# Kernel tuning notes

Hardware: AMD Instinct MI355X
Metric: run time of the kernel (lower is better)

## Reference

```python
import jax, jax.numpy as jnp
import numpy as np

B, N, D, H = 8, 1024, 512, 8
DH = D // H  # one_head_dim = 64


def setup_inputs() -> dict:
    key = jax.random.key(0)
    ks = jax.random.split(key, 7)
    s = 0.02
    return {
        "x": jax.random.normal(ks[0], (B, N, D), dtype=jnp.float32),
        "bias": jax.random.normal(ks[1], (B, N, N, H), dtype=jnp.float32),
        "Wq": jax.random.normal(ks[2], (D, D), dtype=jnp.float32) * s,
        "Wk": jax.random.normal(ks[3], (D, D), dtype=jnp.float32) * s,
        "Wv": jax.random.normal(ks[4], (D, D), dtype=jnp.float32) * s,
        "Wm": jax.random.normal(ks[5], (D, D), dtype=jnp.float32) * s,
        "bm": jnp.zeros((D,), dtype=jnp.float32),
    }


def reference(x, bias, Wq, Wk, Wv, Wm, bm):
    # Linear layers (torch Linear: y = x @ W.T); dropout is identity at eval.
    scale = DH ** -0.5
    q = (x @ Wq.T).reshape(B, N, H, DH).transpose(0, 2, 1, 3) * scale  # [B,H,N,DH]
    k = (x @ Wk.T).reshape(B, N, H, DH).transpose(0, 2, 1, 3)
    v = (x @ Wv.T).reshape(B, N, H, DH).transpose(0, 2, 1, 3)
    # scores + additive pairwise bias (bias permuted [B,N,N,H] -> [B,H,N,N])
    scores = jnp.einsum("bhnd,bhmd->bhnm", q, k) + bias.transpose(0, 3, 1, 2)
    attn = jax.nn.softmax(scores, axis=-1)
    out = jnp.einsum("bhnm,bhmd->bhnd", attn, v)  # [B,H,N,DH]
    out = out.transpose(0, 2, 1, 3).reshape(B, N, D)
    return out @ Wm.T + bm
```

## Files before the change

### kernel.cpp

```cpp
#include <hip/hip_runtime.h>
#include <hip/hip_bf16.h>

typedef __bf16 bf16x8 __attribute__((ext_vector_type(8)));
typedef __bf16 bf16x4 __attribute__((ext_vector_type(4)));
typedef float  f32x4  __attribute__((ext_vector_type(4)));

#define MFMA16(a, b, c) __builtin_amdgcn_mfma_f32_16x16x32_bf16((a), (b), (c), 0, 0, 0)

typedef const __attribute__((address_space(1))) unsigned int* gas_t;
typedef __attribute__((address_space(3))) unsigned int* las_t;
__device__ __forceinline__ void dma16(const __bf16* g, __bf16* l) {
    __builtin_amdgcn_global_load_lds((gas_t)g, (las_t)l, 16, 0, 0);
}


__global__ __launch_bounds__(256) void gemm_qkv(
    const float* __restrict__ x,
    const float* __restrict__ Wq, const float* __restrict__ Wk,
    const float* __restrict__ Wv,
    __bf16* __restrict__ qo, __bf16* __restrict__ ko, __bf16* __restrict__ vto)
{
    __shared__ __bf16 As[64][40];
    __shared__ __bf16 Bs[3][64][40];
    const int tid  = threadIdx.x;
    const int lane = tid & 63;
    const int wid  = tid >> 6;
    const int g    = lane >> 4, l16 = lane & 15;
    const int wr   = wid >> 1,  wc  = wid & 1;
    const int r0   = blockIdx.x * 64;
    const int c0   = blockIdx.y * 64;
    const float* Ws[3] = { Wq, Wk, Wv };

    const int sr  = tid >> 3;
    const int scq = tid & 7;

    f32x4 acc[3][2][2] = {};

    for (int k0 = 0; k0 < 512; k0 += 32) {
        __syncthreads();
#pragma unroll
        for (int j = 0; j < 2; ++j) {
            const int r = sr + 32 * j;
            float4 av = *reinterpret_cast<const float4*>(x + (size_t)(r0 + r) * 512 + k0 + scq * 4);
            bf16x4 ap = { (__bf16)av.x, (__bf16)av.y, (__bf16)av.z, (__bf16)av.w };
            *reinterpret_cast<bf16x4*>(&As[r][scq * 4]) = ap;
#pragma unroll
            for (int widx = 0; widx < 3; ++widx) {
                float4 bv = *reinterpret_cast<const float4*>(Ws[widx] + (size_t)(c0 + r) * 512 + k0 + scq * 4);
                bf16x4 bp = { (__bf16)bv.x, (__bf16)bv.y, (__bf16)bv.z, (__bf16)bv.w };
                *reinterpret_cast<bf16x4*>(&Bs[widx][r][scq * 4]) = bp;
            }
        }
        __syncthreads();
        bf16x8 af[2];
#pragma unroll
        for (int rt = 0; rt < 2; ++rt)
            af[rt] = *reinterpret_cast<const bf16x8*>(&As[wr * 32 + rt * 16 + l16][g * 8]);
#pragma unroll
        for (int widx = 0; widx < 3; ++widx) {
            bf16x8 bfr[2];
#pragma unroll
            for (int ct = 0; ct < 2; ++ct)
                bfr[ct] = *reinterpret_cast<const bf16x8*>(&Bs[widx][wc * 32 + ct * 16 + l16][g * 8]);
#pragma unroll
            for (int rt = 0; rt < 2; ++rt)
#pragma unroll
                for (int ct = 0; ct < 2; ++ct)
                    acc[widx][rt][ct] = MFMA16(af[rt], bfr[ct], acc[widx][rt][ct]);
        }
    }

#pragma unroll
    for (int widx = 0; widx < 2; ++widx) {
        __bf16* dst = (widx == 0) ? qo : ko;
        const float scale = (widx == 0) ? 0.125f : 1.0f;
#pragma unroll
        for (int rt = 0; rt < 2; ++rt)
#pragma unroll
            for (int ct = 0; ct < 2; ++ct)
#pragma unroll
                for (int reg = 0; reg < 4; ++reg) {
                    int r = r0 + wr * 32 + rt * 16 + 4 * g + reg;
                    int c = c0 + wc * 32 + ct * 16 + l16;
                    float val = acc[widx][rt][ct][reg] * scale;
                    int b = r >> 10, n = r & 1023, h = c >> 6, dh = c & 63;
                    dst[(((size_t)b * 8 + h) * 1024 + n) * 64 + dh] = (__bf16)val;
                }
    }
#pragma unroll
    for (int rt = 0; rt < 2; ++rt)
#pragma unroll
        for (int ct = 0; ct < 2; ++ct) {
            int r = r0 + wr * 32 + rt * 16 + 4 * g;
            int c = c0 + wc * 32 + ct * 16 + l16;
            int b = r >> 10, n = r & 1023, h = c >> 6, dh = c & 63;
            bf16x4 pv = { (__bf16)acc[2][rt][ct][0], (__bf16)acc[2][rt][ct][1],
                          (__bf16)acc[2][rt][ct][2], (__bf16)acc[2][rt][ct][3] };
            *reinterpret_cast<bf16x4*>(vto + (((size_t)b * 8 + h) * 64 + dh) * 1024 + n) = pv;
        }
}

__global__ __launch_bounds__(512, 2) void attn_v7(
    const __bf16* __restrict__ qw, const __bf16* __restrict__ kw,
    const __bf16* __restrict__ vtw, const float* __restrict__ bias,
    __bf16* __restrict__ ow)
{
    __shared__ __align__(16) __bf16 Ks[8][32][64];
    __shared__ __align__(16) __bf16 Vs[8][64][32];
    __shared__ __align__(16) __bf16 bsm[2][8][32][36];
    __shared__ __bf16 psm[8][32][40];
    const int tid  = threadIdx.x;
    const int w    = tid >> 6;
    const int lane = tid & 63;
    const int g    = lane >> 4, l16 = lane & 15;
    const int b    = blockIdx.x;
    const int n0   = blockIdx.y * 32;
    const size_t bhs = (size_t)b * 8 + w;

    const __bf16* kbase  = kw  + bhs * 1024 * 64;
    const __bf16* vbase  = vtw + bhs * 64 * 1024;
    const float*  bias_b = bias + ((size_t)(b * 1024 + n0)) * 8192;

    const int snr = tid >> 4;
    const int sf  = tid & 15;

    const int k_row  = lane >> 3;
    const int k_csrc = (lane & 7) ^ (k_row & 7);
    const int v_row  = lane >> 2;
    const int v_mc   = lane & 3;

    bf16x8 qf[2][2];
#pragma unroll
    for (int rf = 0; rf < 2; ++rf)
#pragma unroll
        for (int kc = 0; kc < 2; ++kc)
            qf[rf][kc] = *reinterpret_cast<const bf16x8*>(
                qw + (bhs * 1024 + n0 + rf * 16 + l16) * 64 + kc * 32 + g * 8);

    f32x4 o[2][4] = {};
    float lrun[2][4] = {};

    f32x4 bpA[4], bpB[4];

#define LOAD_BIAS(dst, tt)                                                     \
    {                                                                          \
        const int m0_ = (tt) * 32;                                             \
        _Pragma("unroll")                                                      \
        for (int c = 0; c < 4; ++c)                                            \
            dst[c] = __builtin_nontemporal_load(reinterpret_cast<const f32x4*>(\
                bias_b + (size_t)snr * 8192 + m0_ * 8 + (sf + 16 * c) * 4));   \
    }

#define WRITE_BIAS(buf, src)                                                   \
    {                                                                          \
        _Pragma("unroll")                                                      \
        for (int c = 0; c < 4; ++c) {                                          \
            const int f4 = sf + 16 * c;                                        \
            const int mm = f4 >> 1, h0 = (f4 & 1) * 4;                         \
            bsm[buf][h0 + 0][mm][snr] = (__bf16)src[c].x;                      \
            bsm[buf][h0 + 1][mm][snr] = (__bf16)src[c].y;                      \
            bsm[buf][h0 + 2][mm][snr] = (__bf16)src[c].z;                      \
            bsm[buf][h0 + 3][mm][snr] = (__bf16)src[c].w;                      \
        }                                                                      \
    }

#define DMA_KV(tt)                                                             \
    {                                                                          \
        const int m0_ = (tt) * 32;                                             \
        _Pragma("unroll")                                                      \
        for (int i = 0; i < 4; ++i)                                            \
            dma16(kbase + (size_t)(m0_ + i * 8 + k_row) * 64 + k_csrc * 8,     \
                  &Ks[w][i * 8][0]);                                           \
        _Pragma("unroll")                                                      \
        for (int i = 0; i < 4; ++i)                                            \
            dma16(vbase + (size_t)(i * 16 + v_row) * 1024 + m0_ + v_mc * 8,    \
                  &Vs[w][i * 16][0]);                                          \
    }

    LOAD_BIAS(bpA, 0)
    DMA_KV(0)
    WRITE_BIAS(0, bpA)
    LOAD_BIAS(bpA, 1)
    LOAD_BIAS(bpB, 2)
    asm volatile("s_waitcnt vmcnt(8)");
    __builtin_amdgcn_sched_barrier(0);
    asm volatile("s_waitcnt lgkmcnt(0)");
    __builtin_amdgcn_s_barrier();
    __builtin_amdgcn_sched_barrier(0);

#define ATTN_STEP(t, BUF, bpX)                                                 \
    {                                                                          \
                           \
        bf16x8 kf[2][2], vf[4];                                                \
        _Pragma("unroll")                                                      \
        for (int ct = 0; ct < 2; ++ct)                                         \
            _Pragma("unroll")                                                  \
            for (int kc = 0; kc < 2; ++kc) {                                   \
                const int mrow = ct * 16 + l16;                                \
                kf[ct][kc] = *reinterpret_cast<const bf16x8*>(                 \
                    &Ks[w][mrow][(((kc * 4 + g) ^ (l16 & 7)) * 8)]);           \
            }                                                                  \
        _Pragma("unroll")                                                      \
        for (int oc = 0; oc < 4; ++oc)                                         \
            vf[oc] = *reinterpret_cast<const bf16x8*>(&Vs[w][oc * 16 + l16][g * 8]); \
        bf16x4 bb[2][2];                                                       \
        _Pragma("unroll")                                                      \
        for (int rf = 0; rf < 2; ++rf)                                         \
            _Pragma("unroll")                                                  \
            for (int ct = 0; ct < 2; ++ct)                                     \
                bb[rf][ct] = *reinterpret_cast<const bf16x4*>(                 \
                    &bsm[BUF][w][ct * 16 + l16][rf * 16 + 4 * g]);             \
                     \
        asm volatile("s_waitcnt lgkmcnt(0)");                                  \
        __builtin_amdgcn_sched_barrier(0);                                     \
        DMA_KV((t) + 1 < 32 ? (t) + 1 : 31)                                    \
                                                                     \
        f32x4 s[2][2] = {};                                                    \
        _Pragma("unroll")                                                      \
        for (int rf = 0; rf < 2; ++rf)                                         \
            _Pragma("unroll")                                                  \
            for (int ct = 0; ct < 2; ++ct) {                                   \
                s[rf][ct] = MFMA16(qf[rf][0], kf[ct][0], s[rf][ct]);           \
                s[rf][ct] = MFMA16(qf[rf][1], kf[ct][1], s[rf][ct]);           \
            }                                                                  \
                                                        \
        _Pragma("unroll")                                                      \
        for (int rf = 0; rf < 2; ++rf)                                         \
            _Pragma("unroll")                                                  \
            for (int reg = 0; reg < 4; ++reg) {                                \
                const int nr = rf * 16 + 4 * g + reg;                          \
                float p0 = __expf(s[rf][0][reg] + (float)bb[rf][0][reg] - 16.0f); \
                float p1 = __expf(s[rf][1][reg] + (float)bb[rf][1][reg] - 16.0f); \
                lrun[rf][reg] += p0 + p1;                                      \
                psm[w][nr][l16]      = (__bf16)p0;                             \
                psm[w][nr][16 + l16] = (__bf16)p1;                             \
            }                                                                  \
        bf16x8 pf[2];                                                          \
        _Pragma("unroll")                                                      \
        for (int rf = 0; rf < 2; ++rf)                                         \
            pf[rf] = *reinterpret_cast<const bf16x8*>(&psm[w][rf * 16 + l16][g * 8]); \
        _Pragma("unroll")                                                      \
        for (int rf = 0; rf < 2; ++rf)                                         \
            _Pragma("unroll")                                                  \
            for (int oc = 0; oc < 4; ++oc)                                     \
                o[rf][oc] = MFMA16(pf[rf], vf[oc], o[rf][oc]);                 \
                        \
        WRITE_BIAS((BUF) ^ 1, bpX)                                             \
        LOAD_BIAS(bpX, (t) + 3 < 32 ? (t) + 3 : 31)                            \
                    \
        asm volatile("s_waitcnt vmcnt(4)");                                    \
        __builtin_amdgcn_sched_barrier(0);                                     \
        asm volatile("s_waitcnt lgkmcnt(0)");                                  \
        __builtin_amdgcn_s_barrier();                                          \
        __builtin_amdgcn_sched_barrier(0);                                     \
    }

    for (int t = 0; t < 32; t += 2) {
        ATTN_STEP(t,     0, bpA)
        ATTN_STEP(t + 1, 1, bpB)
    }
#undef ATTN_STEP
#undef LOAD_BIAS
#undef WRITE_BIAS
#undef DMA_KV

#pragma unroll
    for (int rf = 0; rf < 2; ++rf)
#pragma unroll
        for (int reg = 0; reg < 4; ++reg) {
            float l = lrun[rf][reg];
            l += __shfl_xor(l, 1);
            l += __shfl_xor(l, 2);
            l += __shfl_xor(l, 4);
            l += __shfl_xor(l, 8);
            lrun[rf][reg] = l;
        }

#pragma unroll
    for (int rf = 0; rf < 2; ++rf)
#pragma unroll
        for (int oc = 0; oc < 4; ++oc)
#pragma unroll
            for (int reg = 0; reg < 4; ++reg) {
                int n  = n0 + rf * 16 + 4 * g + reg;
                int dh = oc * 16 + l16;
                float val = o[rf][oc][reg] / lrun[rf][reg];
                ow[((size_t)b * 1024 + n) * 512 + w * 64 + dh] = (__bf16)val;
            }
}

__global__ __launch_bounds__(256) void gemm_out(
    const __bf16* __restrict__ a, const float* __restrict__ Wm,
    const float* __restrict__ bm, float* __restrict__ out)
{
    __shared__ __bf16 As[64][40];
    __shared__ __bf16 Bs[64][40];
    const int tid  = threadIdx.x;
    const int lane = tid & 63;
    const int wid  = tid >> 6;
    const int g    = lane >> 4, l16 = lane & 15;
    const int wr   = wid >> 1,  wc  = wid & 1;
    const int r0   = blockIdx.x * 64;
    const int c0   = blockIdx.y * 64;

    const int sra = tid >> 2, sca = tid & 3;
    const int srb = tid >> 3, scb = tid & 7;

    f32x4 acc[2][2] = {};
    for (int k0 = 0; k0 < 512; k0 += 32) {
        __syncthreads();
        {
            bf16x8 av = *reinterpret_cast<const bf16x8*>(a + (size_t)(r0 + sra) * 512 + k0 + sca * 8);
            *reinterpret_cast<bf16x8*>(&As[sra][sca * 8]) = av;
#pragma unroll
            for (int j = 0; j < 2; ++j) {
                int r = srb + 32 * j;
                float4 bv = *reinterpret_cast<const float4*>(Wm + (size_t)(c0 + r) * 512 + k0 + scb * 4);
                bf16x4 bp = { (__bf16)bv.x, (__bf16)bv.y, (__bf16)bv.z, (__bf16)bv.w };
                *reinterpret_cast<bf16x4*>(&Bs[r][scb * 4]) = bp;
            }
        }
        __syncthreads();
        bf16x8 af[2], bfr[2];
#pragma unroll
        for (int rt = 0; rt < 2; ++rt)
            af[rt] = *reinterpret_cast<const bf16x8*>(&As[wr * 32 + rt * 16 + l16][g * 8]);
#pragma unroll
        for (int ct = 0; ct < 2; ++ct)
            bfr[ct] = *reinterpret_cast<const bf16x8*>(&Bs[wc * 32 + ct * 16 + l16][g * 8]);
#pragma unroll
        for (int rt = 0; rt < 2; ++rt)
#pragma unroll
            for (int ct = 0; ct < 2; ++ct)
                acc[rt][ct] = MFMA16(af[rt], bfr[ct], acc[rt][ct]);
    }

#pragma unroll
    for (int rt = 0; rt < 2; ++rt)
#pragma unroll
        for (int ct = 0; ct < 2; ++ct)
#pragma unroll
            for (int reg = 0; reg < 4; ++reg) {
                int r = r0 + wr * 32 + rt * 16 + 4 * g + reg;
                int c = c0 + wc * 32 + ct * 16 + l16;
                out[(size_t)r * 512 + c] = acc[rt][ct][reg] + bm[c];
            }
}

extern "C" void kernel_launch(void* const* d_in, const int* in_sizes, int n_in,
                              void* d_out, int out_size, void* d_ws, size_t ws_size,
                              hipStream_t stream)
{
    const float* x    = (const float*)d_in[0];
    const float* bias = (const float*)d_in[1];
    const float* Wq   = (const float*)d_in[2];
    const float* Wk   = (const float*)d_in[3];
    const float* Wv   = (const float*)d_in[4];
    const float* Wm   = (const float*)d_in[5];
    const float* bm   = (const float*)d_in[6];
    float* out = (float*)d_out;

    const size_t SEG = (size_t)8 * 8 * 1024 * 64;
    __bf16* qw  = (__bf16*)d_ws;
    __bf16* kw  = qw + SEG;
    __bf16* vtw = kw + SEG;
    __bf16* ow  = vtw + SEG;

    gemm_qkv<<<dim3(128, 8), 256, 0, stream>>>(x, Wq, Wk, Wv, qw, kw, vtw);
    attn_v7 <<<dim3(8, 32), 512, 0, stream>>>(qw, kw, vtw, bias, ow);
    gemm_out<<<dim3(128, 8), 256, 0, stream>>>(ow, Wm, bm, out);
}
```

Baseline: 137.9 us.

## Split attention heads across two blocks to double grid size

The attention kernel now handles 4 heads per 256-thread block instead of 8 heads per 512-thread block, which doubles the grid from 256 to 512 blocks. Bias loads are remapped so each thread reads one 16-byte group of 4 heads per key position rather than full 32-byte rows, and shared-memory tiles shrink accordingly. The aim is better occupancy and load balance across the CUs, since 256 blocks is close to one wave on this GPU. The cost is that bias reads become half-row 16-byte strided accesses, so each 32-byte row is split between two blocks, which may reduce coalescing.

```diff
diff --git a/kernel.cpp b/kernel.cpp
--- a/kernel.cpp
+++ b/kernel.cpp
@@ -100,29 +100,31 @@
         }
 }
 
-__global__ __launch_bounds__(512, 2) void attn_v7(
+__global__ __launch_bounds__(256, 2) void attn_v8(
     const __bf16* __restrict__ qw, const __bf16* __restrict__ kw,
     const __bf16* __restrict__ vtw, const float* __restrict__ bias,
     __bf16* __restrict__ ow)
 {
-    __shared__ __align__(16) __bf16 Ks[8][32][64];
-    __shared__ __align__(16) __bf16 Vs[8][64][32];
-    __shared__ __align__(16) __bf16 bsm[2][8][32][36];
-    __shared__ __bf16 psm[8][32][40];
+    __shared__ __align__(16) __bf16 Ks[4][32][64];
+    __shared__ __align__(16) __bf16 Vs[4][64][32];
+    __shared__ __align__(16) __bf16 bsm[2][4][32][36];
+    __shared__ __bf16 psm[4][32][40];
     const int tid  = threadIdx.x;
     const int w    = tid >> 6;
     const int lane = tid & 63;
     const int g    = lane >> 4, l16 = lane & 15;
-    const int b    = blockIdx.x;
+    const int bx   = blockIdx.x;
+    const int b    = bx & 7, hh = bx >> 3;
+    const int h    = hh * 4 + w;
     const int n0   = blockIdx.y * 32;
-    const size_t bhs = (size_t)b * 8 + w;
+    const size_t bhs = (size_t)b * 8 + h;
 
     const __bf16* kbase  = kw  + bhs * 1024 * 64;
     const __bf16* vbase  = vtw + bhs * 64 * 1024;
-    const float*  bias_b = bias + ((size_t)(b * 1024 + n0)) * 8192;
-
-    const int snr = tid >> 4;
-    const int sf  = tid & 15;
+    const float*  bias_b = bias + ((size_t)(b * 1024 + n0)) * 8192 + hh * 4;
+
+    const int snr = tid >> 3;
+    const int sc  = tid & 7;
 
     const int k_row  = lane >> 3;
     const int k_csrc = (lane & 7) ^ (k_row & 7);
@@ -148,19 +150,18 @@
         _Pragma("unroll")                                                      \
         for (int c = 0; c < 4; ++c)                                            \
             dst[c] = __builtin_nontemporal_load(reinterpret_cast<const f32x4*>(\
-                bias_b + (size_t)snr * 8192 + m0_ * 8 + (sf + 16 * c) * 4));   \
+                bias_b + (size_t)snr * 8192 + (size_t)(m0_ + sc + 8 * c) * 8));\
     }
 
 #define WRITE_BIAS(buf, src)                                                   \
     {                                                                          \
         _Pragma("unroll")                                                      \
         for (int c = 0; c < 4; ++c) {                                          \
-            const int f4 = sf + 16 * c;                                        \
-            const int mm = f4 >> 1, h0 = (f4 & 1) * 4;                         \
-            bsm[buf][h0 + 0][mm][snr] = (__bf16)src[c].x;                      \
-            bsm[buf][h0 + 1][mm][snr] = (__bf16)src[c].y;                      \
-            bsm[buf][h0 + 2][mm][snr] = (__bf16)src[c].z;                      \
-            bsm[buf][h0 + 3][mm][snr] = (__bf16)src[c].w;                      \
+            const int mm = sc + 8 * c;                                         \
+            bsm[buf][0][mm][snr] = (__bf16)src[c].x;                           \
+            bsm[buf][1][mm][snr] = (__bf16)src[c].y;                           \
+            bsm[buf][2][mm][snr] = (__bf16)src[c].z;                           \
+            bsm[buf][3][mm][snr] = (__bf16)src[c].w;                           \
         }                                                                      \
     }
 
@@ -190,7 +191,6 @@
 
 #define ATTN_STEP(t, BUF, bpX)                                                 \
     {                                                                          \
-                           \
         bf16x8 kf[2][2], vf[4];                                                \
         _Pragma("unroll")                                                      \
         for (int ct = 0; ct < 2; ++ct)                                         \
@@ -210,11 +210,9 @@
             for (int ct = 0; ct < 2; ++ct)                                     \
                 bb[rf][ct] = *reinterpret_cast<const bf16x4*>(                 \
                     &bsm[BUF][w][ct * 16 + l16][rf * 16 + 4 * g]);             \
-                     \
         asm volatile("s_waitcnt lgkmcnt(0)");                                  \
         __builtin_amdgcn_sched_barrier(0);                                     \
         DMA_KV((t) + 1 < 32 ? (t) + 1 : 31)                                    \
-                                                                     \
         f32x4 s[2][2] = {};                                                    \
         _Pragma("unroll")                                                      \
         for (int rf = 0; rf < 2; ++rf)                                         \
@@ -223,7 +221,6 @@
                 s[rf][ct] = MFMA16(qf[rf][0], kf[ct][0], s[rf][ct]);           \
                 s[rf][ct] = MFMA16(qf[rf][1], kf[ct][1], s[rf][ct]);           \
             }                                                                  \
-                                                        \
         _Pragma("unroll")                                                      \
         for (int rf = 0; rf < 2; ++rf)                                         \
             _Pragma("unroll")                                                  \
@@ -244,10 +241,8 @@
             _Pragma("unroll")                                                  \
             for (int oc = 0; oc < 4; ++oc)                                     \
                 o[rf][oc] = MFMA16(pf[rf], vf[oc], o[rf][oc]);                 \
-                        \
         WRITE_BIAS((BUF) ^ 1, bpX)                                             \
         LOAD_BIAS(bpX, (t) + 3 < 32 ? (t) + 3 : 31)                            \
-                    \
         asm volatile("s_waitcnt vmcnt(4)");                                    \
         __builtin_amdgcn_sched_barrier(0);                                     \
         asm volatile("s_waitcnt lgkmcnt(0)");                                  \
@@ -285,7 +280,7 @@
                 int n  = n0 + rf * 16 + 4 * g + reg;
                 int dh = oc * 16 + l16;
                 float val = o[rf][oc][reg] / lrun[rf][reg];
-                ow[((size_t)b * 1024 + n) * 512 + w * 64 + dh] = (__bf16)val;
+                ow[((size_t)b * 1024 + n) * 512 + h * 64 + dh] = (__bf16)val;
             }
 }
 
@@ -367,6 +362,6 @@
     __bf16* ow  = vtw + SEG;
 
     gemm_qkv<<<dim3(128, 8), 256, 0, stream>>>(x, Wq, Wk, Wv, qw, kw, vtw);
-    attn_v7 <<<dim3(8, 32), 512, 0, stream>>>(qw, kw, vtw, bias, ow);
+    attn_v8 <<<dim3(16, 32), 256, 0, stream>>>(qw, kw, vtw, bias, ow);
     gemm_out<<<dim3(128, 8), 256, 0, stream>>>(ow, Wm, bm, out);
 }
```

Measured after the change: 149.1 us. +8.1%, slower.

## Halve attention query tile, load V directly to registers, raise occupancy

Applied to the files above, without the earlier changes.

The attention kernel now processes 16 query rows per block instead of 32, doubling the grid to 512 blocks and raising launch bounds to 4 blocks per CU. V tiles are loaded from global memory straight into registers with double buffering instead of going through LDS via DMA, and the bias prefetch depth drops from three tiles to two. The intent is more parallelism and latency hiding on the bias-bandwidth-bound kernel. The cost is that each K and V tile is now reloaded by twice as many blocks, which doubles K/V traffic per query row.

```diff
diff --git a/kernel.cpp b/kernel.cpp
--- a/kernel.cpp
+++ b/kernel.cpp
@@ -100,98 +100,98 @@
         }
 }
 
-__global__ __launch_bounds__(512, 2) void attn_v7(
+__global__ __launch_bounds__(512, 4) void attn_v9(
     const __bf16* __restrict__ qw, const __bf16* __restrict__ kw,
     const __bf16* __restrict__ vtw, const float* __restrict__ bias,
     __bf16* __restrict__ ow)
 {
     __shared__ __align__(16) __bf16 Ks[8][32][64];
-    __shared__ __align__(16) __bf16 Vs[8][64][32];
-    __shared__ __align__(16) __bf16 bsm[2][8][32][36];
-    __shared__ __bf16 psm[8][32][40];
+    __shared__ __align__(16) __bf16 bsm[2][8][32][20];
+    __shared__ __bf16 psm[8][16][40];
     const int tid  = threadIdx.x;
     const int w    = tid >> 6;
     const int lane = tid & 63;
     const int g    = lane >> 4, l16 = lane & 15;
     const int b    = blockIdx.x;
-    const int n0   = blockIdx.y * 32;
+    const int n0   = blockIdx.y * 16;
     const size_t bhs = (size_t)b * 8 + w;
 
     const __bf16* kbase  = kw  + bhs * 1024 * 64;
     const __bf16* vbase  = vtw + bhs * 64 * 1024;
     const float*  bias_b = bias + ((size_t)(b * 1024 + n0)) * 8192;
 
-    const int snr = tid >> 4;
-    const int sf  = tid & 15;
+    const int snr = tid >> 5;
+    const int sf  = tid & 31;
 
     const int k_row  = lane >> 3;
     const int k_csrc = (lane & 7) ^ (k_row & 7);
-    const int v_row  = lane >> 2;
-    const int v_mc   = lane & 3;
-
-    bf16x8 qf[2][2];
-#pragma unroll
-    for (int rf = 0; rf < 2; ++rf)
-#pragma unroll
-        for (int kc = 0; kc < 2; ++kc)
-            qf[rf][kc] = *reinterpret_cast<const bf16x8*>(
-                qw + (bhs * 1024 + n0 + rf * 16 + l16) * 64 + kc * 32 + g * 8);
-
-    f32x4 o[2][4] = {};
-    float lrun[2][4] = {};
-
-    f32x4 bpA[4], bpB[4];
-
-#define LOAD_BIAS(dst, tt)                                                     \
+
+    bf16x8 qf[2];
+#pragma unroll
+    for (int kc = 0; kc < 2; ++kc)
+        qf[kc] = *reinterpret_cast<const bf16x8*>(
+            qw + (bhs * 1024 + n0 + l16) * 64 + kc * 32 + g * 8);
+
+    f32x4 o[4] = {};
+    float lrun[4] = {};
+
+    f32x4  bp[2];
+    bf16x8 vpA[4], vpB[4];
+
+#define LOAD_BIAS(tt)                                                          \
     {                                                                          \
         const int m0_ = (tt) * 32;                                             \
         _Pragma("unroll")                                                      \
-        for (int c = 0; c < 4; ++c)                                            \
-            dst[c] = __builtin_nontemporal_load(reinterpret_cast<const f32x4*>(\
-                bias_b + (size_t)snr * 8192 + m0_ * 8 + (sf + 16 * c) * 4));   \
-    }
-
-#define WRITE_BIAS(buf, src)                                                   \
-    {                                                                          \
-        _Pragma("unroll")                                                      \
-        for (int c = 0; c < 4; ++c) {                                          \
-            const int f4 = sf + 16 * c;                                        \
+        for (int c = 0; c < 2; ++c)                                            \
+            bp[c] = __builtin_nontemporal_load(reinterpret_cast<const f32x4*>( \
+                bias_b + (size_t)snr * 8192 + m0_ * 8 + (sf + 32 * c) * 4));   \
+    }
+
+#define WRITE_BIAS(buf)                                                        \
+    {                                                                          \
+        _Pragma("unroll")                                                      \
+        for (int c = 0; c < 2; ++c) {                                          \
+            const int f4 = sf + 32 * c;                                        \
             const int mm = f4 >> 1, h0 = (f4 & 1) * 4;                         \
-            bsm[buf][h0 + 0][mm][snr] = (__bf16)src[c].x;                      \
-            bsm[buf][h0 + 1][mm][snr] = (__bf16)src[c].y;                      \
-            bsm[buf][h0 + 2][mm][snr] = (__bf16)src[c].z;                      \
-            bsm[buf][h0 + 3][mm][snr] = (__bf16)src[c].w;                      \
+            bsm[buf][h0 + 0][mm][snr] = (__bf16)bp[c].x;                       \
+            bsm[buf][h0 + 1][mm][snr] = (__bf16)bp[c].y;                       \
+            bsm[buf][h0 + 2][mm][snr] = (__bf16)bp[c].z;                       \
+            bsm[buf][h0 + 3][mm][snr] = (__bf16)bp[c].w;                       \
         }                                                                      \
     }
 
-#define DMA_KV(tt)                                                             \
+#define DMA_K(tt)                                                              \
     {                                                                          \
         const int m0_ = (tt) * 32;                                             \
         _Pragma("unroll")                                                      \
         for (int i = 0; i < 4; ++i)                                            \
             dma16(kbase + (size_t)(m0_ + i * 8 + k_row) * 64 + k_csrc * 8,     \
                   &Ks[w][i * 8][0]);                                           \
-        _Pragma("unroll")                                                      \
-        for (int i = 0; i < 4; ++i)                                            \
-            dma16(vbase + (size_t)(i * 16 + v_row) * 1024 + m0_ + v_mc * 8,    \
-                  &Vs[w][i * 16][0]);                                          \
-    }
-
-    LOAD_BIAS(bpA, 0)
-    DMA_KV(0)
-    WRITE_BIAS(0, bpA)
-    LOAD_BIAS(bpA, 1)
-    LOAD_BIAS(bpB, 2)
-    asm volatile("s_waitcnt vmcnt(8)");
+    }
+
+#define LOAD_V(dst, tt)                                                        \
+    {                                                                          \
+        const int m0_ = (tt) * 32;                                             \
+        _Pragma("unroll")                                                      \
+        for (int oc = 0; oc < 4; ++oc)                                         \
+            dst[oc] = *reinterpret_cast<const bf16x8*>(                        \
+                vbase + (size_t)(oc * 16 + l16) * 1024 + m0_ + g * 8);         \
+    }
+
+    LOAD_BIAS(0)
+    DMA_K(0)
+    LOAD_V(vpA, 0)
+    WRITE_BIAS(0)
+    LOAD_BIAS(1)
+    asm volatile("s_waitcnt vmcnt(6)");
     __builtin_amdgcn_sched_barrier(0);
     asm volatile("s_waitcnt lgkmcnt(0)");
     __builtin_amdgcn_s_barrier();
     __builtin_amdgcn_sched_barrier(0);
 
-#define ATTN_STEP(t, BUF, bpX)                                                 \
-    {                                                                          \
-                           \
-        bf16x8 kf[2][2], vf[4];                                                \
+#define ATTN_STEP(t, BUF, VCUR, VNXT)                                          \
+    {                                                                          \
+        bf16x8 kf[2][2];                                                       \
         _Pragma("unroll")                                                      \
         for (int ct = 0; ct < 2; ++ct)                                         \
             _Pragma("unroll")                                                  \
@@ -200,55 +200,43 @@
                 kf[ct][kc] = *reinterpret_cast<const bf16x8*>(                 \
                     &Ks[w][mrow][(((kc * 4 + g) ^ (l16 & 7)) * 8)]);           \
             }                                                                  \
-        _Pragma("unroll")                                                      \
-        for (int oc = 0; oc < 4; ++oc)                                         \
-            vf[oc] = *reinterpret_cast<const bf16x8*>(&Vs[w][oc * 16 + l16][g * 8]); \
-        bf16x4 bb[2][2];                                                       \
-        _Pragma("unroll")                                                      \
-        for (int rf = 0; rf < 2; ++rf)                                         \
-            _Pragma("unroll")                                                  \
-            for (int ct = 0; ct < 2; ++ct)                                     \
-                bb[rf][ct] = *reinterpret_cast<const bf16x4*>(                 \
-                    &bsm[BUF][w][ct * 16 + l16][rf * 16 + 4 * g]);             \
-                     \
+        bf16x4 bb[2];                                                          \
+        _Pragma("unroll")                                                      \
+        for (int ct = 0; ct < 2; ++ct)                                         \
+            bb[ct] = *reinterpret_cast<const bf16x4*>(                         \
+                &bsm[BUF][w][ct * 16 + l16][4 * g]);                           \
+                          \
         asm volatile("s_waitcnt lgkmcnt(0)");                                  \
         __builtin_amdgcn_sched_barrier(0);                                     \
-        DMA_KV((t) + 1 < 32 ? (t) + 1 : 31)                                    \
+        DMA_K((t) + 1 < 32 ? (t) + 1 : 31)                                     \
+        LOAD_V(VNXT, (t) + 1 < 32 ? (t) + 1 : 31)                              \
                                                                      \
-        f32x4 s[2][2] = {};                                                    \
-        _Pragma("unroll")                                                      \
-        for (int rf = 0; rf < 2; ++rf)                                         \
-            _Pragma("unroll")                                                  \
-            for (int ct = 0; ct < 2; ++ct) {                                   \
-                s[rf][ct] = MFMA16(qf[rf][0], kf[ct][0], s[rf][ct]);           \
-                s[rf][ct] = MFMA16(qf[rf][1], kf[ct][1], s[rf][ct]);           \
-            }                                                                  \
+        f32x4 s[2] = {};                                                       \
+        _Pragma("unroll")                                                      \
+        for (int ct = 0; ct < 2; ++ct) {                                       \
+            s[ct] = MFMA16(qf[0], kf[ct][0], s[ct]);                           \
+            s[ct] = MFMA16(qf[1], kf[ct][1], s[ct]);                           \
+        }                                                                      \
                                                         \
         _Pragma("unroll")                                                      \
-        for (int rf = 0; rf < 2; ++rf)                                         \
-            _Pragma("unroll")                                                  \
-            for (int reg = 0; reg < 4; ++reg) {                                \
-                const int nr = rf * 16 + 4 * g + reg;                          \
-                float p0 = __expf(s[rf][0][reg] + (float)bb[rf][0][reg] - 16.0f); \
-                float p1 = __expf(s[rf][1][reg] + (float)bb[rf][1][reg] - 16.0f); \
-                lrun[rf][reg] += p0 + p1;                                      \
-                psm[w][nr][l16]      = (__bf16)p0;                             \
-                psm[w][nr][16 + l16] = (__bf16)p1;                             \
-            }                                                                  \
-        bf16x8 pf[2];                                                          \
-        _Pragma("unroll")                                                      \
-        for (int rf = 0; rf < 2; ++rf)                                         \
-            pf[rf] = *reinterpret_cast<const bf16x8*>(&psm[w][rf * 16 + l16][g * 8]); \
-        _Pragma("unroll")                                                      \
-        for (int rf = 0; rf < 2; ++rf)                                         \
-            _Pragma("unroll")                                                  \
-            for (int oc = 0; oc < 4; ++oc)                                     \
-                o[rf][oc] = MFMA16(pf[rf], vf[oc], o[rf][oc]);                 \
+        for (int reg = 0; reg < 4; ++reg) {                                    \
+            const int nr = 4 * g + reg;                                        \
+            float p0 = __expf(s[0][reg] + (float)bb[0][reg] - 16.0f);          \
+            float p1 = __expf(s[1][reg] + (float)bb[1][reg] - 16.0f);          \
+            lrun[reg] += p0 + p1;                                              \
+            psm[w][nr][l16]      = (__bf16)p0;                                 \
+            psm[w][nr][16 + l16] = (__bf16)p1;                                 \
+        }                                                                      \
+        asm volatile("s_waitcnt lgkmcnt(0)");                                  \
+        __builtin_amdgcn_sched_barrier(0);                                     \
+        bf16x8 pf = *reinterpret_cast<const bf16x8*>(&psm[w][l16][g * 8]);     \
+        _Pragma("unroll")                                                      \
+        for (int oc = 0; oc < 4; ++oc)                                         \
+            o[oc] = MFMA16(pf, VCUR[oc], o[oc]);                               \
                         \
-        WRITE_BIAS((BUF) ^ 1, bpX)                                             \
-        LOAD_BIAS(bpX, (t) + 3 < 32 ? (t) + 3 : 31)                            \
-                    \
-        asm volatile("s_waitcnt vmcnt(4)");                                    \
+        WRITE_BIAS((BUF) ^ 1)                                                  \
+        LOAD_BIAS((t) + 2 < 32 ? (t) + 2 : 31)                                 \
+        asm volatile("s_waitcnt vmcnt(6)");      \
         __builtin_amdgcn_sched_barrier(0);                                     \
         asm volatile("s_waitcnt lgkmcnt(0)");                                  \
         __builtin_amdgcn_s_barrier();                                          \
@@ -256,37 +244,34 @@
     }
 
     for (int t = 0; t < 32; t += 2) {
-        ATTN_STEP(t,     0, bpA)
-        ATTN_STEP(t + 1, 1, bpB)
+        ATTN_STEP(t,     0, vpA, vpB)
+        ATTN_STEP(t + 1, 1, vpB, vpA)
     }
 #undef ATTN_STEP
 #undef LOAD_BIAS
 #undef WRITE_BIAS
-#undef DMA_KV
-
-#pragma unroll
-    for (int rf = 0; rf < 2; ++rf)
+#undef DMA_K
+#undef LOAD_V
+
+#pragma unroll
+    for (int reg = 0; reg < 4; ++reg) {
+        float l = lrun[reg];
+        l += __shfl_xor(l, 1);
+        l += __shfl_xor(l, 2);
+        l += __shfl_xor(l, 4);
+        l += __shfl_xor(l, 8);
+        lrun[reg] = l;
+    }
+
+#pragma unroll
+    for (int oc = 0; oc < 4; ++oc)
 #pragma unroll
         for (int reg = 0; reg < 4; ++reg) {
-            float l = lrun[rf][reg];
-            l += __shfl_xor(l, 1);
-            l += __shfl_xor(l, 2);
-            l += __shfl_xor(l, 4);
-            l += __shfl_xor(l, 8);
-            lrun[rf][reg] = l;
-        }
-
-#pragma unroll
-    for (int rf = 0; rf < 2; ++rf)
-#pragma unroll
-        for (int oc = 0; oc < 4; ++oc)
-#pragma unroll
-            for (int reg = 0; reg < 4; ++reg) {
-                int n  = n0 + rf * 16 + 4 * g + reg;
-                int dh = oc * 16 + l16;
-                float val = o[rf][oc][reg] / lrun[rf][reg];
-                ow[((size_t)b * 1024 + n) * 512 + w * 64 + dh] = (__bf16)val;
-            }
+            int n  = n0 + 4 * g + reg;
+            int dh = oc * 16 + l16;
+            float val = o[oc][reg] / lrun[reg];
+            ow[((size_t)b * 1024 + n) * 512 + w * 64 + dh] = (__bf16)val;
+        }
 }
 
 __global__ __launch_bounds__(256) void gemm_out(
@@ -367,6 +352,6 @@
     __bf16* ow  = vtw + SEG;
 
     gemm_qkv<<<dim3(128, 8), 256, 0, stream>>>(x, Wq, Wk, Wv, qw, kw, vtw);
-    attn_v7 <<<dim3(8, 32), 512, 0, stream>>>(qw, kw, vtw, bias, ow);
+    attn_v9 <<<dim3(8, 64), 512, 0, stream>>>(qw, kw, vtw, bias, ow);
     gemm_out<<<dim3(128, 8), 256, 0, stream>>>(ow, Wm, bm, out);
 }
```

After: 165.0 us. +19.7%, slower.
